# Kernel tuning notes

Measured on AMD Instinct MI355X. Metric: run time of the kernel, lower is better.

Reference implementation:

```python
import math
import jax, jax.numpy as jnp
import numpy as np

B, N, D, NC, TMAX = 8, 4096, 1024, 512, 1000


def setup_inputs() -> dict:
    key = jax.random.key(0)
    ks = jax.random.split(key, 12)
    tokens = jax.random.normal(ks[0], (B, N, D), jnp.float32)
    ctx_C = jax.random.normal(ks[1], (B, NC, D), jnp.float32)
    t = jax.random.randint(ks[2], (B,), 0, TMAX, dtype=jnp.int32)
    rare_mask = jax.random.bernoulli(ks[3], 0.05, (B, N))
    # Linear params stored as (in, out); scaled so scores straddle 0.5
    ctx_w = jax.random.normal(ks[4], (D, D // 4), jnp.float32) / math.sqrt(D)
    ctx_b = jax.random.normal(ks[5], (D // 4,), jnp.float32) * 0.01
    t_proj_w = jax.random.normal(ks[6], (D, D), jnp.float32) / math.sqrt(D)
    t_proj_b = jax.random.normal(ks[7], (D,), jnp.float32) * 0.01
    HIN = D + D // 4 + D  # 2304
    w1 = jax.random.normal(ks[8], (HIN, D // 2), jnp.float32) / math.sqrt(HIN)
    b1 = jax.random.normal(ks[9], (D // 2,), jnp.float32) * 0.01
    w2 = jax.random.normal(ks[10], (D // 2,), jnp.float32) * 0.1
    b2 = jnp.zeros((1,), jnp.float32)
    return {"tokens": tokens, "ctx_C": ctx_C, "t": t, "rare_mask": rare_mask,
            "ctx_w": ctx_w, "ctx_b": ctx_b, "t_proj_w": t_proj_w,
            "t_proj_b": t_proj_b, "w1": w1, "b1": b1, "w2": w2, "b2": b2}


def reference(tokens, ctx_C, t, rare_mask, ctx_w, ctx_b, t_proj_w, t_proj_b, w1, b1, w2, b2):
    Bb, Nn, Dd = tokens.shape
    half = Dd // 2
    # sinusoidal timestep embedding buffer (matches torch register_buffer)
    freq = jnp.exp(-math.log(10000.0) * jnp.arange(half, dtype=jnp.float32) / max(half - 1, 1))
    # bottlenecked context: mean over ctx tokens -> (B, D//4)
    ctx_bn = ctx_C.mean(axis=1) @ ctx_w + ctx_b
    args = t.astype(jnp.float32)[:, None] * freq[None, :]            # (B, half)
    emb = jnp.concatenate([jnp.sin(args), jnp.cos(args)], axis=-1)   # (B, D)
    t_emb = emb @ t_proj_w + t_proj_b                                # (B, D)
    x = jnp.concatenate([
        tokens,
        jnp.broadcast_to(ctx_bn[:, None, :], (Bb, Nn, Dd // 4)),
        jnp.broadcast_to(t_emb[:, None, :], (Bb, Nn, Dd)),
    ], axis=-1)                                                       # (B, N, 2.25D)
    h = jax.nn.relu(x @ w1 + b1)                                      # (B, N, D//2)
    scores = jax.nn.sigmoid(h @ w2 + b2)                              # (B, N)
    skip = (scores > 0.5) & jnp.logical_not(rare_mask)
    min_active = max(1, int(Nn * 0.2))
    active = jnp.logical_not(skip).sum(axis=-1)                       # (B,)
    deficit = jnp.maximum(min_active - active, 0)                     # (B,)
    masked = jnp.where(skip, scores, jnp.inf)
    rank = jnp.argsort(jnp.argsort(masked, axis=-1), axis=-1)         # rank among skipped, ascending score
    skip = skip & jnp.logical_not(rank < deficit[:, None])
    return skip, scores
```

## Files before the change

kernel.cpp:

```cpp
#include <hip/hip_runtime.h>
#include <math.h>

#define NN 4096
#define DD 1024
#define M_TOT 32768
#define H1 512
#define MIN_ACTIVE 819
#define MARGIN 0.03f
#define MAXFIX 8192

typedef __bf16 bf16x8 __attribute__((ext_vector_type(8)));
typedef float f32x4 __attribute__((ext_vector_type(4)));

__device__ __forceinline__ unsigned short f2bf(float f) {
    unsigned int u = __float_as_uint(f);
    return (unsigned short)((u + 0x7FFFu + ((u >> 16) & 1u)) >> 16);
}

__device__ __forceinline__ void glds16(const unsigned short* g, unsigned short* l) {
    __builtin_amdgcn_global_load_lds(
        (const __attribute__((address_space(1))) unsigned int*)g,
        (__attribute__((address_space(3))) unsigned int*)l, 16, 0, 0);
}

__global__ void convB_pmean_kernel(const float* __restrict__ w1, unsigned short* __restrict__ w1tt,
                                   const float* __restrict__ ctx, float* __restrict__ pmean,
                                   const unsigned char* __restrict__ rare, int* __restrict__ mode,
                                   int* __restrict__ fixcnt) {
    __shared__ float tile[32][65];
    __shared__ int nonbin, oneoff;
    int blk = blockIdx.x;
    int tid = threadIdx.x;
    if (blk < 256) {
        int t = blk >> 3;
        int c0 = (blk & 7) * 64;
        #pragma unroll
        for (int i = 0; i < 8; ++i) {
            int idx = tid + 256 * i;
            int kk = idx >> 6, cc = idx & 63;
            tile[kk][cc] = w1[(size_t)(t * 32 + kk) * H1 + c0 + cc];
        }
        __syncthreads();
        {
            int cc = tid >> 2, jp = tid & 3;
            int c = c0 + cc;
            int j = jp ^ ((c >> 1) & 3);
            unsigned int w[4];
            #pragma unroll
            for (int q = 0; q < 4; ++q)
                w[q] = (unsigned int)f2bf(tile[j * 8 + 2 * q][cc])
                     | ((unsigned int)f2bf(tile[j * 8 + 2 * q + 1][cc]) << 16);
            uint4 v; v.x = w[0]; v.y = w[1]; v.z = w[2]; v.w = w[3];
            *(uint4*)(w1tt + ((size_t)t * 512 + c) * 32 + jp * 8) = v;
        }
        if (blk == 0) {
            if (tid == 0) { nonbin = 0; oneoff = 0; *fixcnt = 0; }
            __syncthreads();
            int lnon = 0, lone = 0;
            for (int i = tid; i < 32768; i += 256) {
                unsigned char b = rare[i];
                if (b > 1) lnon = 1;
                else if (b == 1 && (i & 3) != 0) lone = 1;
            }
            if (lnon) atomicOr(&nonbin, 1);
            if (lone) atomicOr(&oneoff, 1);
            __syncthreads();
            if (tid == 0) *mode = nonbin ? 2 : (oneoff ? 1 : 0);
        }
    } else {
        int pblk = blk - 256;
        int b = pblk >> 5, dq = (pblk >> 3) & 3, nz = pblk & 7;
        int d = dq * 256 + tid;
        const float* base = ctx + ((size_t)(b * 512 + nz * 64)) * DD + d;
        float acc = 0.f;
        for (int n = 0; n < 64; ++n) acc += base[(size_t)n * DD];
        pmean[(b * 8 + nz) * DD + d] = acc;
    }
}

__global__ void prep_kernel(const float* __restrict__ pmean, const int* __restrict__ t,
                            float* __restrict__ mean, float* __restrict__ embf) {
    int idx = blockIdx.x * 256 + threadIdx.x;
    int b = idx >> 10, j = idx & 1023;
    float s = 0.f;
    for (int nz = 0; nz < 8; ++nz) s += pmean[(b * 8 + nz) * DD + j];
    mean[idx] = s * (1.f / 512.f);
    int jj = j & 511;
    double arg = (double)t[b] * exp((-log(10000.0) / 511.0) * (double)jj);
    embf[idx] = (float)((j < 512) ? sin(arg) : cos(arg));
}

__global__ __launch_bounds__(256) void midk_kernel(
    const float* __restrict__ mean, const float* __restrict__ embf,
    const float* __restrict__ ctx_w, const float* __restrict__ ctx_b,
    const float* __restrict__ tpw, const float* __restrict__ tpb,
    float* __restrict__ ctx_bn, float* __restrict__ t_emb) {
    __shared__ float red8[8][32];
    __shared__ float red4[4][64];
    int tid = threadIdx.x;
    if (blockIdx.x < 64) {
        int b = blockIdx.x >> 3, cg = blockIdx.x & 7;
        int c = cg * 32 + (tid & 31), ks = tid >> 5;
        const float* mb = mean + b * DD + ks * 128;
        const float* wb = ctx_w + (size_t)(ks * 128) * 256 + c;
        float acc = 0.f;
        for (int i = 0; i < 128; ++i) acc += mb[i] * wb[(size_t)i * 256];
        red8[ks][tid & 31] = acc;
        __syncthreads();
        if (tid < 32) {
            float s = 0.f;
            for (int k = 0; k < 8; ++k) s += red8[k][tid];
            ctx_bn[b * 256 + cg * 32 + tid] = s + ctx_b[cg * 32 + tid];
        }
    } else {
        int blk = blockIdx.x - 64;
        int b = blk >> 4, cg = blk & 15;
        int c = cg * 64 + (tid & 63), ks = tid >> 6;
        const float* eb = embf + b * DD + ks * 256;
        const float* wb = tpw + (size_t)(ks * 256) * DD + c;
        float acc = 0.f;
        for (int i = 0; i < 256; ++i) acc += eb[i] * wb[(size_t)i * DD];
        red4[ks][tid & 63] = acc;
        __syncthreads();
        if (tid < 64) {
            float s = red4[0][tid] + red4[1][tid] + red4[2][tid] + red4[3][tid];
            t_emb[b * DD + cg * 64 + tid] = s + tpb[cg * 64 + tid];
        }
    }
}

__global__ void baseh_kernel(const float* __restrict__ ctx_bn, const float* __restrict__ t_emb,
                             const float* __restrict__ w1, const float* __restrict__ b1,
                             float* __restrict__ base_h) {
    __shared__ float red[8][32];
    int b = blockIdx.x, cg = blockIdx.y;
    int c = cg * 32 + (threadIdx.x & 31), ks = threadIdx.x >> 5;
    float acc = 0.f;
    for (int i = 0; i < 160; ++i) {
        int k = ks * 160 + i;
        float v = (k < 256) ? ctx_bn[b * 256 + k] : t_emb[b * DD + k - 256];
        acc += v * w1[(size_t)(1024 + k) * H1 + c];
    }
    red[ks][threadIdx.x & 31] = acc;
    __syncthreads();
    if (threadIdx.x < 32) {
        float s = 0.f;
        for (int k = 0; k < 8; ++k) s += red[k][threadIdx.x];
        base_h[b * H1 + cg * 32 + threadIdx.x] = s + b1[cg * 32 + threadIdx.x];
    }
}

__global__ __launch_bounds__(512, 4) void gemm_kernel(
    const float* __restrict__ tokens, const unsigned short* __restrict__ w1tt,
    const float* __restrict__ baseh, const float* __restrict__ w2,
    float* __restrict__ part) {
    __shared__ unsigned short As[2][128 * 40];
    __shared__ unsigned short Bs[2][256 * 32];
    __shared__ float red[128][4];
    int tid = threadIdx.x;
    int lane = tid & 63, wid = tid >> 6;
    int wm = wid >> 2, wn = wid & 3;
    int la = lane & 15, lk = lane >> 4;
    int row0 = blockIdx.x * 128;
    int half = blockIdx.y;
    const unsigned short* wsrc = w1tt + (size_t)half * 256 * 32;

    f32x4 acc[4][4];
    #pragma unroll
    for (int i = 0; i < 4; ++i)
        #pragma unroll
        for (int j = 0; j < 4; ++j)
            acc[i][j] = (f32x4){0.f, 0.f, 0.f, 0.f};

    float4 sa[2];
    #define LOAD_A(kt_) { \
        _Pragma("unroll") \
        for (int i = 0; i < 2; ++i) { \
            int id = tid + 512 * i; \
            int r = id >> 3, xk = id & 7; \
            sa[i] = *(const float4*)(tokens + (size_t)(row0 + r) * DD + (kt_) + xk * 4); \
        } }
    #define WRITE_A(bb_) { \
        _Pragma("unroll") \
        for (int i = 0; i < 2; ++i) { \
            int id = tid + 512 * i; \
            int r = id >> 3, xk = id & 7; \
            ushort4 h; \
            h.x = f2bf(sa[i].x); h.y = f2bf(sa[i].y); \
            h.z = f2bf(sa[i].z); h.w = f2bf(sa[i].w); \
            *(ushort4*)(&As[bb_][r * 40 + xk * 4]) = h; \
        } }
    #define STAGE_B(t_, bb_) { \
        const unsigned short* gsrc = wsrc + (size_t)(t_) * 512 * 32; \
        _Pragma("unroll") \
        for (int q = 0; q < 2; ++q) { \
            int chunk = wid * 2 + q; \
            glds16(gsrc + chunk * 512 + lane * 8, &Bs[bb_][chunk * 512]); \
        } }

    STAGE_B(0, 0);
    LOAD_A(0);
    WRITE_A(0);
    LOAD_A(32);
    asm volatile("s_waitcnt lgkmcnt(0)" ::: "memory");
    __builtin_amdgcn_s_barrier();
    __builtin_amdgcn_sched_barrier(0);

    for (int t = 0; t < 32; ++t) {
        int bb = t & 1;
        bf16x8 af[4], bfr[4];
        #pragma unroll
        for (int mf = 0; mf < 4; ++mf) {
            int r = wm * 64 + mf * 16 + la;
            af[mf] = *(const bf16x8*)(&As[bb][r * 40 + lk * 8]);
        }
        #pragma unroll
        for (int nf = 0; nf < 4; ++nf) {
            int c = wn * 64 + nf * 16 + la;
            int sw = lk ^ ((c >> 1) & 3);
            bfr[nf] = *(const bf16x8*)(&Bs[bb][c * 32 + sw * 8]);
        }
        if (t < 31) {
            WRITE_A(bb ^ 1);
            STAGE_B(t + 1, bb ^ 1);
            __builtin_amdgcn_sched_barrier(0);
            if (t < 30) LOAD_A((t + 2) * 32);
        }
        #pragma unroll
        for (int mf = 0; mf < 4; ++mf)
            #pragma unroll
            for (int nf = 0; nf < 4; ++nf)
                acc[mf][nf] = __builtin_amdgcn_mfma_f32_16x16x32_bf16(af[mf], bfr[nf], acc[mf][nf], 0, 0, 0);
        if (t < 31) {
            if (t < 30) asm volatile("s_waitcnt vmcnt(2)" ::: "memory");
            else        asm volatile("s_waitcnt vmcnt(0)" ::: "memory");
            asm volatile("s_waitcnt lgkmcnt(0)" ::: "memory");
            __builtin_amdgcn_s_barrier();
            __builtin_amdgcn_sched_barrier(0);
        }
    }
    #undef LOAD_A
    #undef WRITE_A
    #undef STAGE_B

    int b = row0 >> 12;
    const float* bh = baseh + b * H1;
    float bhv[4], w2v[4];
    #pragma unroll
    for (int nf = 0; nf < 4; ++nf) {
        int col = half * 256 + wn * 64 + nf * 16 + la;
        bhv[nf] = bh[col];
        w2v[nf] = w2[col];
    }
    #pragma unroll
    for (int mf = 0; mf < 4; ++mf) {
        #pragma unroll
        for (int reg = 0; reg < 4; ++reg) {
            float p = 0.f;
            #pragma unroll
            for (int nf = 0; nf < 4; ++nf) {
                float h = acc[mf][nf][reg] + bhv[nf];
                h = fmaxf(h, 0.f);
                p += h * w2v[nf];
            }
            p += __shfl_xor(p, 1, 64);
            p += __shfl_xor(p, 2, 64);
            p += __shfl_xor(p, 4, 64);
            p += __shfl_xor(p, 8, 64);
            if (la == 0) red[wm * 64 + mf * 16 + lk * 4 + reg][wn] = p;
        }
    }
    __syncthreads();
    if (tid < 128)
        part[(size_t)(row0 + tid) * 2 + half] = red[tid][0] + red[tid][1] + red[tid][2] + red[tid][3];
}

__global__ void score_kernel(const float* __restrict__ part, const float* __restrict__ b2,
                             const void* __restrict__ rare, const int* __restrict__ mode_p,
                             float* __restrict__ out, int* __restrict__ fixcnt,
                             int* __restrict__ fixlist) {
    int row = blockIdx.x * 256 + threadIdx.x;
    float logit = part[(size_t)row * 2] + part[(size_t)row * 2 + 1] + b2[0];
    float score = 1.f / (1.f + expf(-logit));
    int mode = *mode_p;
    bool rm = (mode == 1) ? (((const unsigned char*)rare)[row] != 0)
            : (mode == 2) ? (((const float*)rare)[row] != 0.f)
            : (((const int*)rare)[row] != 0);
    out[row] = ((score > 0.5f) && !rm) ? 1.f : 0.f;
    out[M_TOT + row] = score;
    if (fabsf(logit) < MARGIN) {
        int i = atomicAdd(fixcnt, 1);
        if (i < MAXFIX) fixlist[i] = row;
    }
}

__global__ __launch_bounds__(512) void fixup_kernel(
    const int* __restrict__ fixcnt, const int* __restrict__ fixlist,
    const float* __restrict__ tokens, const float* __restrict__ w1,
    const float* __restrict__ base_h, const float* __restrict__ w2,
    const float* __restrict__ b2, const void* __restrict__ rare,
    const int* __restrict__ mode_p, float* __restrict__ out) {
    __shared__ float tok[DD];
    __shared__ float part4[4][H1];
    __shared__ float red[8];
    int tid = threadIdx.x;
    int lane = tid & 63, wid = tid >> 6;
    int ks = tid >> 7;
    int cg = tid & 127;
    int n = *fixcnt;
    if (n > MAXFIX) n = MAXFIX;
    for (int g = blockIdx.x; g < n; g += gridDim.x) {
        int row = fixlist[g];
        int b = row >> 12;
        if (tid < 256)
            ((float4*)tok)[tid] = ((const float4*)(tokens + (size_t)row * DD))[tid];
        __syncthreads();
        const float* wbase = w1 + (size_t)(ks * 256) * H1 + cg * 4;
        const float* tbase = tok + ks * 256;
        float4 a = {0.f, 0.f, 0.f, 0.f};
        #pragma unroll 8
        for (int k = 0; k < 256; ++k) {
            float4 w = *(const float4*)(wbase + (size_t)k * H1);
            float tv = tbase[k];
            a.x += tv * w.x; a.y += tv * w.y; a.z += tv * w.z; a.w += tv * w.w;
        }
        *(float4*)&part4[ks][cg * 4] = a;
        __syncthreads();
        float h = part4[0][tid] + part4[1][tid] + part4[2][tid] + part4[3][tid]
                + base_h[b * H1 + tid];
        h = fmaxf(h, 0.f);
        float p = h * w2[tid];
        p += __shfl_xor(p, 1, 64);
        p += __shfl_xor(p, 2, 64);
        p += __shfl_xor(p, 4, 64);
        p += __shfl_xor(p, 8, 64);
        p += __shfl_xor(p, 16, 64);
        p += __shfl_xor(p, 32, 64);
        if (lane == 0) red[wid] = p;
        __syncthreads();
        if (tid == 0) {
            float logit = b2[0];
            #pragma unroll
            for (int w = 0; w < 8; ++w) logit += red[w];
            float score = 1.f / (1.f + expf(-logit));
            int mode = *mode_p;
            bool rm = (mode == 1) ? (((const unsigned char*)rare)[row] != 0)
                    : (mode == 2) ? (((const float*)rare)[row] != 0.f)
                    : (((const int*)rare)[row] != 0);
            out[row] = ((score > 0.5f) && !rm) ? 1.f : 0.f;
            out[M_TOT + row] = score;
        }
        __syncthreads();
    }
}

__global__ void floor_kernel(float* __restrict__ out) {
    __shared__ float s[NN];
    __shared__ unsigned char f[NN];
    __shared__ int cnt;
    int b = blockIdx.x, tid = threadIdx.x;
    if (tid == 0) cnt = 0;
    __syncthreads();
    int local = 0;
    for (int i = tid; i < NN; i += 256) {
        s[i] = out[M_TOT + b * NN + i];
        unsigned char sk = out[b * NN + i] > 0.5f;
        f[i] = sk;
        local += sk;
    }
    atomicAdd(&cnt, local);
    __syncthreads();
    int deficit = cnt - (NN - MIN_ACTIVE);
    if (deficit <= 0) return;
    for (int i = tid; i < NN; i += 256) {
        if (!f[i]) continue;
        float si = s[i];
        int rank = 0;
        for (int j = 0; j < NN; ++j) {
            if (f[j] && (s[j] < si || (s[j] == si && j < i))) {
                if (++rank >= deficit) break;
            }
        }
        if (rank < deficit) out[b * NN + i] = 0.f;
    }
}

extern "C" void kernel_launch(void* const* d_in, const int* in_sizes, int n_in,
                              void* d_out, int out_size, void* d_ws, size_t ws_size,
                              hipStream_t stream) {
    const float* tokens   = (const float*)d_in[0];
    const float* ctx_C    = (const float*)d_in[1];
    const int*   t        = (const int*)d_in[2];
    const void*  rare     = d_in[3];
    const float* ctx_w    = (const float*)d_in[4];
    const float* ctx_b    = (const float*)d_in[5];
    const float* t_proj_w = (const float*)d_in[6];
    const float* t_proj_b = (const float*)d_in[7];
    const float* w1       = (const float*)d_in[8];
    const float* b1       = (const float*)d_in[9];
    const float* w2       = (const float*)d_in[10];
    const float* b2       = (const float*)d_in[11];
    float* out = (float*)d_out;

    char* ws = (char*)d_ws;
    unsigned short* w1tt  = (unsigned short*)(ws);
    float* pmean          = (float*)(ws + 1048576);
    float* part           = (float*)(ws + 1048576);
    float* mean           = (float*)(ws + 1310720);
    float* embf           = (float*)(ws + 1343488);
    float* ctx_bn         = (float*)(ws + 1376256);
    float* t_emb          = (float*)(ws + 1384448);
    float* base_h         = (float*)(ws + 1417216);
    int*   mode           = (int*)  (ws + 1433600);
    int*   fixcnt         = (int*)  (ws + 1433664);
    int*   fixlist        = (int*)  (ws + 1433728);

    convB_pmean_kernel<<<512, 256, 0, stream>>>(w1, w1tt, ctx_C, pmean,
                                                (const unsigned char*)rare, mode, fixcnt);
    prep_kernel<<<32, 256, 0, stream>>>(pmean, t, mean, embf);
    midk_kernel<<<192, 256, 0, stream>>>(mean, embf, ctx_w, ctx_b, t_proj_w, t_proj_b, ctx_bn, t_emb);
    baseh_kernel<<<dim3(8, 16), 256, 0, stream>>>(ctx_bn, t_emb, w1, b1, base_h);
    gemm_kernel<<<dim3(256, 2), 512, 0, stream>>>(tokens, w1tt, base_h, w2, part);
    score_kernel<<<128, 256, 0, stream>>>(part, b2, rare, mode, out, fixcnt, fixlist);
    fixup_kernel<<<512, 512, 0, stream>>>(fixcnt, fixlist, tokens, w1, base_h, w2, b2, rare, mode, out);
    floor_kernel<<<8, 256, 0, stream>>>(out);
}
```

Before: 176.3 us.

## Triple-buffer B tiles with two-stage prefetch and raise MFMA wave priority

The weight tile buffer in shared memory grows from two stages to three, so B tiles are fetched two iterations ahead. The token tile now alternates between two register buffers so its global loads also run two steps ahead. Loads are issued after the MFMA block instead of before it, and the wait loosens to vmcnt(4). s_setprio brackets the MFMA loop so compute waves get issue priority. The cost is more LDS per block, which may limit occupancy, and more registers for the second A buffer.

```diff
diff --git a/kernel.cpp b/kernel.cpp
--- a/kernel.cpp
+++ b/kernel.cpp
@@ -155,7 +155,7 @@
     const float* __restrict__ baseh, const float* __restrict__ w2,
     float* __restrict__ part) {
     __shared__ unsigned short As[2][128 * 40];
-    __shared__ unsigned short Bs[2][256 * 32];
+    __shared__ unsigned short Bs[3][256 * 32];
     __shared__ float red[128][4];
     int tid = threadIdx.x;
     int lane = tid & 63, wid = tid >> 6;
@@ -172,22 +172,22 @@
         for (int j = 0; j < 4; ++j)
             acc[i][j] = (f32x4){0.f, 0.f, 0.f, 0.f};
 
-    float4 sa[2];
-    #define LOAD_A(kt_) { \
+    float4 sa0[2], sa1[2];
+    #define LOAD_A(kt_, S_) { \
         _Pragma("unroll") \
         for (int i = 0; i < 2; ++i) { \
             int id = tid + 512 * i; \
             int r = id >> 3, xk = id & 7; \
-            sa[i] = *(const float4*)(tokens + (size_t)(row0 + r) * DD + (kt_) + xk * 4); \
+            S_[i] = *(const float4*)(tokens + (size_t)(row0 + r) * DD + (kt_) + xk * 4); \
         } }
-    #define WRITE_A(bb_) { \
+    #define WRITE_A(bb_, S_) { \
         _Pragma("unroll") \
         for (int i = 0; i < 2; ++i) { \
             int id = tid + 512 * i; \
             int r = id >> 3, xk = id & 7; \
             ushort4 h; \
-            h.x = f2bf(sa[i].x); h.y = f2bf(sa[i].y); \
-            h.z = f2bf(sa[i].z); h.w = f2bf(sa[i].w); \
+            h.x = f2bf(S_[i].x); h.y = f2bf(S_[i].y); \
+            h.z = f2bf(S_[i].z); h.w = f2bf(S_[i].w); \
             *(ushort4*)(&As[bb_][r * 40 + xk * 4]) = h; \
         } }
     #define STAGE_B(t_, bb_) { \
@@ -198,16 +198,20 @@
             glds16(gsrc + chunk * 512 + lane * 8, &Bs[bb_][chunk * 512]); \
         } }
 
+    LOAD_A(0, sa0);
     STAGE_B(0, 0);
-    LOAD_A(0);
-    WRITE_A(0);
-    LOAD_A(32);
+    STAGE_B(1, 1);
+    WRITE_A(0, sa0);
+    LOAD_A(32, sa1);
+    __builtin_amdgcn_sched_barrier(0);
+    asm volatile("s_waitcnt vmcnt(4)" ::: "memory");
     asm volatile("s_waitcnt lgkmcnt(0)" ::: "memory");
     __builtin_amdgcn_s_barrier();
     __builtin_amdgcn_sched_barrier(0);
 
     for (int t = 0; t < 32; ++t) {
         int bb = t & 1;
+        const unsigned short* bsrc = Bs[t % 3];
         bf16x8 af[4], bfr[4];
         #pragma unroll
         for (int mf = 0; mf < 4; ++mf) {
@@ -218,21 +222,24 @@
         for (int nf = 0; nf < 4; ++nf) {
             int c = wn * 64 + nf * 16 + la;
             int sw = lk ^ ((c >> 1) & 3);
-            bfr[nf] = *(const bf16x8*)(&Bs[bb][c * 32 + sw * 8]);
-        }
-        if (t < 31) {
-            WRITE_A(bb ^ 1);
-            STAGE_B(t + 1, bb ^ 1);
-            __builtin_amdgcn_sched_barrier(0);
-            if (t < 30) LOAD_A((t + 2) * 32);
-        }
+            bfr[nf] = *(const bf16x8*)(&bsrc[c * 32 + sw * 8]);
+        }
+        __builtin_amdgcn_s_setprio(1);
         #pragma unroll
         for (int mf = 0; mf < 4; ++mf)
             #pragma unroll
             for (int nf = 0; nf < 4; ++nf)
                 acc[mf][nf] = __builtin_amdgcn_mfma_f32_16x16x32_bf16(af[mf], bfr[nf], acc[mf][nf], 0, 0, 0);
+        __builtin_amdgcn_s_setprio(0);
+        __builtin_amdgcn_sched_barrier(0);
         if (t < 31) {
-            if (t < 30) asm volatile("s_waitcnt vmcnt(2)" ::: "memory");
+            if (t & 1) { WRITE_A(bb ^ 1, sa0) } else { WRITE_A(bb ^ 1, sa1) }
+            if (t < 30) {
+                if (t & 1) { LOAD_A((t + 2) * 32, sa1) } else { LOAD_A((t + 2) * 32, sa0) }
+                STAGE_B(t + 2, (t + 2) % 3);
+            }
+            __builtin_amdgcn_sched_barrier(0);
+            if (t < 30) asm volatile("s_waitcnt vmcnt(4)" ::: "memory");
             else        asm volatile("s_waitcnt vmcnt(0)" ::: "memory");
             asm volatile("s_waitcnt lgkmcnt(0)" ::: "memory");
             __builtin_amdgcn_s_barrier();
```

Result: no change. 177.9 us (+0.9%).
